# Kernel optimization log

Measured on AMD Instinct MI355X. Metric: run time of the kernel, lower is better.

Reference implementation:

```python
import jax, jax.numpy as jnp
import numpy as np

_D4_CODESZ = 4
_NUM_SCALE = 1024.0


def _code3_signs(i3, x):
    if i3 & (1 << 5):
        x[2] *= -1
    if i3 & (1 << 6):
        x[1] *= -1
    if sum(x) % 2 != 0:
        x[3] *= -1
    if i3 & (1 << 7):
        x = [-v for v in x]
    assert sum(x) % 2 == 0
    return x


def _code8_to_d4(i8):
    assert 0 <= i8 < 256
    i3 = i8 & (7 << 5)
    i8 = i8 & 31
    if i8 < 16:
        if i8 < 8:
            if i8 < 2:
                if i8 < 1:
                    return _code3_signs(i3, [0.5] * _D4_CODESZ)
                else:
                    return _code3_signs(i3, [1.5] * _D4_CODESZ)
            else:
                ibx = i8 >> 1
                if i8 & 1:
                    x = [0.5] * _D4_CODESZ
                    x[0] = 1.5
                    x[ibx] = 1.5
                else:
                    x = [1.5] * _D4_CODESZ
                    x[0] = 0.5
                    x[ibx] = 0.5
                return _code3_signs(i3, x)
        else:
            ibx = i8 & 3
            if i8 < 8 + 4:
                x = [0.5] * _D4_CODESZ
                x[ibx] = 1.5
            else:
                x = [1.5] * _D4_CODESZ
                x[ibx] = 0.5
            return _code3_signs(i3, x)
    elif i8 < 16 + 4:
        ibx = i8 & 3
        x = [0.5] * _D4_CODESZ
        x[ibx] = 2.5
        return _code3_signs(i3, x)
    else:
        ibx = i8 - 20
        ib4 = ibx & 3
        ib3 = ibx >> 2
        x = [0.5] * _D4_CODESZ
        x[ib4] = 1.5
        if ib3 >= ib4:
            ib3 += 1
        x[ib3] = 2.5
        return _code3_signs(i3, x)


def build_d4_cb():
    cb = np.zeros((256, _D4_CODESZ), dtype=np.float32)
    for i in range(256):
        cb[i] = _code8_to_d4(i)
    return jnp.asarray(cb, dtype=jnp.float16)


def fwht(x):
    """Normalized fast Walsh-Hadamard transform over the last axis (power of 2).
    The normalized Hadamard matrix is symmetric, so U and U^T coincide."""
    shp = x.shape
    n = shp[-1]
    x = x.reshape(-1, n)
    h = 1
    while h < n:
        x = x.reshape(-1, n // (2 * h), 2, h)
        a = x[:, :, 0, :]
        b = x[:, :, 1, :]
        x = jnp.stack([a + b, a - b], axis=2).reshape(-1, n)
        h *= 2
    return (x * np.float32(1.0 / np.sqrt(n))).reshape(shp)


def setup_inputs() -> dict:
    key = jax.random.key(0)
    k1, k2, k3, k4, k5 = jax.random.split(key, 5)
    m, n = 4096, 1024  # out_features=m, in_features=4*n
    d_in = _D4_CODESZ * n
    inp = {
        "input": jax.random.normal(k1, (4, 2048, d_in), dtype=jnp.float32),
        "Qidxs": jax.random.randint(k2, (m, n), 0, 256, dtype=jnp.int32),
        "SU": jnp.sign(jax.random.normal(k3, (d_in,), dtype=jnp.float32)),
        "SV": jnp.sign(jax.random.normal(k4, (m,), dtype=jnp.float32)),
        "Wscale": jax.random.uniform(k5, (1,), dtype=jnp.float32) + 0.5,
        "D4_CB": build_d4_cb(),
    }
    return inp


def reference(input, Qidxs, SU, SV, Wscale, D4_CB):
    m, n = Qidxs.shape
    d_in = _D4_CODESZ * n
    x = input.reshape(-1, d_in).astype(jnp.float32)  # [T, 4n]
    x = x * SU                                        # sign diag
    x = fwht(x)                                       # AutogradOrthoMult, transpose=1
    x = (x / _NUM_SCALE).astype(jnp.float16)
    # on-the-fly D4 dequant: gather codebook rows, fuse into GEMM
    W = D4_CB[Qidxs].reshape(m, d_in)                 # [m, 4n] fp16
    z = x @ W.T                                       # [T, m] fp16 (AutogradQuip)
    x = z.astype(jnp.float32) * (Wscale * _NUM_SCALE)
    x = fwht(x)                                       # AutogradOrthoMult, transpose=0
    x = x * SV                                        # sign diag
    return x.reshape(input.shape[:-1] + (m,))
```

## Files before the change

### kernel.cpp

```cpp
#include <hip/hip_runtime.h>
#include <hip/hip_fp16.h>

typedef _Float16 half8 __attribute__((ext_vector_type(8)));
typedef _Float16 half4v __attribute__((ext_vector_type(4)));
typedef float floatx4 __attribute__((ext_vector_type(4)));

#define K_DIM 4096
#define N_DIM 4096
#define B_ROWS 8192

#define BM 256
#define BN 256
#define BK 64
#define NTILES (K_DIM / BK)

__global__ __launch_bounds__(256) void decode_kernel(
    const int* __restrict__ qidxs, const float4* __restrict__ cb,
    half4v* __restrict__ w) {
  int i = blockIdx.x * 256 + threadIdx.x;
  float4 v = cb[qidxs[i]];
  half4v h;
  h.x = (_Float16)v.x;
  h.y = (_Float16)v.y;
  h.z = (_Float16)v.z;
  h.w = (_Float16)v.w;
  w[i] = h;
}

__global__ __launch_bounds__(256) void fwht_in_kernel(
    const float* __restrict__ x, const float* __restrict__ su,
    _Float16* __restrict__ out) {
  __shared__ float s[4096];
  const int t = threadIdx.x;
  const float4* xv = (const float4*)(x + (size_t)blockIdx.x * 4096);
  const float4* uv = (const float4*)su;
  for (int i = t; i < 1024; i += 256) {
    float4 v = xv[i], u = uv[i];
    s[4 * i + 0] = v.x * u.x;
    s[4 * i + 1] = v.y * u.y;
    s[4 * i + 2] = v.z * u.z;
    s[4 * i + 3] = v.w * u.w;
  }
  __syncthreads();
  for (int h = 1; h < 4096; h <<= 1) {
    for (int j = t; j < 2048; j += 256) {
      int idx = ((j & ~(h - 1)) << 1) | (j & (h - 1));
      float a = s[idx], b = s[idx + h];
      s[idx] = a + b;
      s[idx + h] = a - b;
    }
    __syncthreads();
  }
  const float sc = 1.0f / 65536.0f;
  half4v* ov = (half4v*)(out + (size_t)blockIdx.x * 4096);
  for (int i = t; i < 1024; i += 256) {
    half4v h4;
    h4.x = (_Float16)(s[4 * i + 0] * sc);
    h4.y = (_Float16)(s[4 * i + 1] * sc);
    h4.z = (_Float16)(s[4 * i + 2] * sc);
    h4.w = (_Float16)(s[4 * i + 3] * sc);
    ov[i] = h4;
  }
}

__device__ __forceinline__ void gload16(const _Float16* g, _Float16* l) {
  __builtin_amdgcn_global_load_lds(
      (const __attribute__((address_space(1))) void*)g,
      (__attribute__((address_space(3))) void*)l, 16, 0, 0);
}

#define MF(a, b, c) __builtin_amdgcn_mfma_f32_16x16x32_f16(a, b, c, 0, 0, 0)

#define LDA(BUFI, M, KS) \
  (*(const half8*)&sA[BUFI][wm * 128 + (M) * 16 + fr][fc ^ ((KS) << 5)])
#define LDB(BUFI, Nn, KS) \
  (*(const half8*)&sB[BUFI][wn * 64 + (Nn) * 16 + fr][fc ^ ((KS) << 5)])

#define STAGE_A(BUFI, HALF, TILE)                                            \
  {                                                                          \
    const _Float16* s_ = gA + (long)(HALF) * 128 * K_DIM + (long)(TILE)*BK;  \
    _Float16* d_ = &sA[BUFI][(HALF)*128 + sr][scl];                          \
    gload16(s_, d_);                                                         \
    gload16(s_ + 64 * (long)K_DIM, d_ + 64 * BK);                            \
  }
#define STAGE_B(BUFI, HALF, TILE)                                            \
  {                                                                          \
    const _Float16* s_ = gB + (long)(HALF) * 128 * K_DIM + (long)(TILE)*BK;  \
    _Float16* d_ = &sB[BUFI][(HALF)*128 + sr][scl];                          \
    gload16(s_, d_);                                                         \
    gload16(s_ + 64 * (long)K_DIM, d_ + 64 * BK);                            \
  }

#define WAIT4 asm volatile("s_waitcnt vmcnt(4)" ::: "memory")
#define WAIT0 asm volatile("s_waitcnt vmcnt(0)" ::: "memory")

#define PHASE(BUFI, M0, STAGE_STMT, TAIL_STMT)                               \
  {                                                                          \
    half8 x00 = LDA(BUFI, M0, 0);                                            \
    half8 x01 = LDA(BUFI, M0, 1);                                            \
    half8 x10 = LDA(BUFI, (M0) + 1, 0);                                      \
    half8 x11 = LDA(BUFI, (M0) + 1, 1);                                      \
    STAGE_STMT;                                                              \
    __builtin_amdgcn_s_barrier();                                            \
    asm volatile("s_waitcnt lgkmcnt(0)" ::: "memory");                       \
    __builtin_amdgcn_sched_barrier(0);                                       \
    __builtin_amdgcn_s_setprio(1);                                           \
    acc[M0][0] = MF(x00, bf[0][0], acc[M0][0]);                              \
    acc[M0][0] = MF(x01, bf[0][1], acc[M0][0]);                              \
    acc[M0][1] = MF(x00, bf[1][0], acc[M0][1]);                              \
    acc[M0][1] = MF(x01, bf[1][1], acc[M0][1]);                              \
    acc[M0][2] = MF(x00, bf[2][0], acc[M0][2]);                              \
    acc[M0][2] = MF(x01, bf[2][1], acc[M0][2]);                              \
    acc[M0][3] = MF(x00, bf[3][0], acc[M0][3]);                              \
    acc[M0][3] = MF(x01, bf[3][1], acc[M0][3]);                              \
    acc[(M0) + 1][0] = MF(x10, bf[0][0], acc[(M0) + 1][0]);                  \
    acc[(M0) + 1][0] = MF(x11, bf[0][1], acc[(M0) + 1][0]);                  \
    acc[(M0) + 1][1] = MF(x10, bf[1][0], acc[(M0) + 1][1]);                  \
    acc[(M0) + 1][1] = MF(x11, bf[1][1], acc[(M0) + 1][1]);                  \
    acc[(M0) + 1][2] = MF(x10, bf[2][0], acc[(M0) + 1][2]);                  \
    acc[(M0) + 1][2] = MF(x11, bf[2][1], acc[(M0) + 1][2]);                  \
    acc[(M0) + 1][3] = MF(x10, bf[3][0], acc[(M0) + 1][3]);                  \
    acc[(M0) + 1][3] = MF(x11, bf[3][1], acc[(M0) + 1][3]);                  \
    __builtin_amdgcn_s_setprio(0);                                           \
    TAIL_STMT;                                                               \
    __builtin_amdgcn_s_barrier();                                            \
  }

#define TILE(BUFI, S1, S2, S3, S4, TAILW)                                    \
  {                                                                          \
    half8 bf[4][2];                                                          \
    bf[0][0] = LDB(BUFI, 0, 0);                                              \
    bf[0][1] = LDB(BUFI, 0, 1);                                              \
    bf[1][0] = LDB(BUFI, 1, 0);                                              \
    bf[1][1] = LDB(BUFI, 1, 1);                                              \
    bf[2][0] = LDB(BUFI, 2, 0);                                              \
    bf[2][1] = LDB(BUFI, 2, 1);                                              \
    bf[3][0] = LDB(BUFI, 3, 0);                                              \
    bf[3][1] = LDB(BUFI, 3, 1);                                              \
    PHASE(BUFI, 0, S1, ;)                                                    \
    PHASE(BUFI, 2, S2, ;)                                                    \
    PHASE(BUFI, 4, S3, ;)                                                    \
    PHASE(BUFI, 6, S4, TAILW)                                                \
  }

__global__ __launch_bounds__(512) void gemm_kernel(
    const _Float16* __restrict__ A,
    const _Float16* __restrict__ B,
    float* __restrict__ C) {
  __shared__ _Float16 sA[2][BM][BK];
  __shared__ _Float16 sB[2][BN][BK];
  const int t = threadIdx.x;
  const int lane = t & 63;
  const int wave = t >> 6;
  const int wm = wave >> 2;
  const int wn = wave & 3;

  const int bid = blockIdx.x;
  const int wg = (bid & 7) * 64 + (bid >> 3);
  const long bm = (long)(wg >> 4) * BM;
  const long bn = (long)(wg & 15) * BN;

  floatx4 acc[8][4];
#pragma unroll
  for (int i = 0; i < 8; i++)
#pragma unroll
    for (int j = 0; j < 4; j++) acc[i][j] = floatx4{0.f, 0.f, 0.f, 0.f};

  const int sr = t >> 3;
  const int scl = (t & 7) << 3;
  const int sc = ((t & 7) ^ (sr & 7)) << 3;
  const _Float16* gA = A + (bm + sr) * (long)K_DIM + sc;
  const _Float16* gB = B + (bn + sr) * (long)K_DIM + sc;

  const int fr = lane & 15;
  const int fc = (((lane >> 4) ^ (lane & 7)) << 3);

  STAGE_A(0, 0, 0);
  STAGE_A(0, 1, 0);
  STAGE_B(0, 0, 0);
  STAGE_B(0, 1, 0);
  STAGE_B(1, 0, 1);
  STAGE_B(1, 1, 1);
  WAIT4;
  __builtin_amdgcn_s_barrier();

#pragma unroll 1
  for (int kt = 0; kt < NTILES - 2; kt += 2) {
    TILE(0, STAGE_A(1, 0, kt + 1), STAGE_A(1, 1, kt + 1),
         STAGE_B(0, 0, kt + 2), STAGE_B(0, 1, kt + 2), WAIT4)
    TILE(1, STAGE_A(0, 0, kt + 2), STAGE_A(0, 1, kt + 2),
         STAGE_B(1, 0, kt + 3), STAGE_B(1, 1, kt + 3), WAIT4)
  }
  TILE(0, STAGE_A(1, 0, NTILES - 1), STAGE_A(1, 1, NTILES - 1), ;, ;, WAIT0)
  TILE(1, ;, ;, ;, ;, ;)

  const int cn = lane & 15;
  const int cm4 = (lane >> 4) << 2;
#pragma unroll
  for (int m = 0; m < 8; m++) {
    const long row0 = bm + wm * 128 + m * 16 + cm4;
#pragma unroll
    for (int n = 0; n < 4; n++) {
      const long col = bn + wn * 64 + n * 16 + cn;
#pragma unroll
      for (int r = 0; r < 4; r++)
        C[(row0 + r) * (long)N_DIM + col] = (float)(_Float16)acc[m][n][r];
    }
  }
}

__global__ __launch_bounds__(256) void fwht_out_kernel(
    float* __restrict__ z, const float* __restrict__ sv,
    const float* __restrict__ wscale) {
  __shared__ float s[4096];
  const int t = threadIdx.x;
  float4* zv = (float4*)(z + (size_t)blockIdx.x * 4096);
  for (int i = t; i < 1024; i += 256) {
    float4 v = zv[i];
    s[4 * i + 0] = v.x;
    s[4 * i + 1] = v.y;
    s[4 * i + 2] = v.z;
    s[4 * i + 3] = v.w;
  }
  __syncthreads();
  for (int h = 1; h < 4096; h <<= 1) {
    for (int j = t; j < 2048; j += 256) {
      int idx = ((j & ~(h - 1)) << 1) | (j & (h - 1));
      float a = s[idx], b = s[idx + h];
      s[idx] = a + b;
      s[idx + h] = a - b;
    }
    __syncthreads();
  }
  const float sc = wscale[0] * 16.0f;
  const float4* svv = (const float4*)sv;
  for (int i = t; i < 1024; i += 256) {
    float4 u = svv[i];
    float4 o;
    o.x = s[4 * i + 0] * sc * u.x;
    o.y = s[4 * i + 1] * sc * u.y;
    o.z = s[4 * i + 2] * sc * u.z;
    o.w = s[4 * i + 3] * sc * u.w;
    zv[i] = o;
  }
}

extern "C" void kernel_launch(void* const* d_in, const int* in_sizes, int n_in,
                              void* d_out, int out_size, void* d_ws, size_t ws_size,
                              hipStream_t stream) {
  const float* input = (const float*)d_in[0];
  const int* qidxs = (const int*)d_in[1];
  const float* su = (const float*)d_in[2];
  const float* sv = (const float*)d_in[3];
  const float* wscale = (const float*)d_in[4];
  const float4* cb = (const float4*)d_in[5];
  float* out = (float*)d_out;

  if (ws_size < 100663296ull) return;
  char* ws = (char*)d_ws;
  _Float16* W16 = (_Float16*)ws;
  _Float16* Xh = (_Float16*)(ws + 33554432ull);

  decode_kernel<<<(4096 * 1024) / 256, 256, 0, stream>>>(qidxs, cb,
                                                         (half4v*)W16);
  fwht_in_kernel<<<B_ROWS, 256, 0, stream>>>(input, su, Xh);
  gemm_kernel<<<dim3((B_ROWS / BM) * (N_DIM / BN)), 512, 0, stream>>>(Xh, W16,
                                                                      out);
  fwht_out_kernel<<<B_ROWS, 256, 0, stream>>>(out, sv, wscale);
}
```

Before: 553.8 us.

## Restructure FWHT kernels as register radix-16 stages, widen decode, reorder MFMAs

Both FWHT kernels now run the 4096-point transform as three radix-16 passes. Each thread holds 16 values in registers, and data moves through an XOR-swizzled shared-memory tile between passes, so only two barriers are needed instead of twelve shared-memory butterfly stages. The decode kernel handles two codebook indices per thread and writes 16-byte vectors. The GEMM MFMA sequence is reordered so that dependent accumulations on the same accumulator are spaced apart. The aim is to cut shared-memory traffic and barrier cost in the memory-bound transform kernels, at the cost of more register use per thread.

Result: faster. 508.1 us (-8.2%).

```diff
diff --git a/kernel.cpp b/kernel.cpp
--- a/kernel.cpp
+++ b/kernel.cpp
@@ -15,52 +15,76 @@
 #define NTILES (K_DIM / BK)
 
 __global__ __launch_bounds__(256) void decode_kernel(
-    const int* __restrict__ qidxs, const float4* __restrict__ cb,
-    half4v* __restrict__ w) {
+    const int2* __restrict__ qidxs, const float4* __restrict__ cb,
+    half8* __restrict__ w) {
   int i = blockIdx.x * 256 + threadIdx.x;
-  float4 v = cb[qidxs[i]];
-  half4v h;
-  h.x = (_Float16)v.x;
-  h.y = (_Float16)v.y;
-  h.z = (_Float16)v.z;
-  h.w = (_Float16)v.w;
+  int2 q = qidxs[i];
+  float4 v0 = cb[q.x];
+  float4 v1 = cb[q.y];
+  half8 h;
+  h[0] = (_Float16)v0.x;
+  h[1] = (_Float16)v0.y;
+  h[2] = (_Float16)v0.z;
+  h[3] = (_Float16)v0.w;
+  h[4] = (_Float16)v1.x;
+  h[5] = (_Float16)v1.y;
+  h[6] = (_Float16)v1.z;
+  h[7] = (_Float16)v1.w;
   w[i] = h;
+}
+
+__device__ __forceinline__ void fwht16(float v[16]) {
+#pragma unroll
+  for (int h = 1; h < 16; h <<= 1) {
+#pragma unroll
+    for (int g = 0; g < 16; g += 2 * h) {
+#pragma unroll
+      for (int j = g; j < g + h; ++j) {
+        float a = v[j], b = v[j + h];
+        v[j] = a + b;
+        v[j + h] = a - b;
+      }
+    }
+  }
 }
 
 __global__ __launch_bounds__(256) void fwht_in_kernel(
     const float* __restrict__ x, const float* __restrict__ su,
     _Float16* __restrict__ out) {
-  __shared__ float s[4096];
+  __shared__ float s[16][264];
   const int t = threadIdx.x;
-  const float4* xv = (const float4*)(x + (size_t)blockIdx.x * 4096);
-  const float4* uv = (const float4*)su;
-  for (int i = t; i < 1024; i += 256) {
-    float4 v = xv[i], u = uv[i];
-    s[4 * i + 0] = v.x * u.x;
-    s[4 * i + 1] = v.y * u.y;
-    s[4 * i + 2] = v.z * u.z;
-    s[4 * i + 3] = v.w * u.w;
+  const float* xr = x + (size_t)blockIdx.x * 4096;
+  float v[16];
+#pragma unroll
+  for (int a = 0; a < 16; ++a) v[a] = xr[a * 256 + t] * su[a * 256 + t];
+  fwht16(v);
+  {
+    const int c = t >> 4, d = t & 15;
+    const int col = c * 16 + (d ^ c);
+#pragma unroll
+    for (int a = 0; a < 16; ++a) s[a][col] = v[a];
   }
   __syncthreads();
-  for (int h = 1; h < 4096; h <<= 1) {
-    for (int j = t; j < 2048; j += 256) {
-      int idx = ((j & ~(h - 1)) << 1) | (j & (h - 1));
-      float a = s[idx], b = s[idx + h];
-      s[idx] = a + b;
-      s[idx + h] = a - b;
-    }
-    __syncthreads();
-  }
+  const int a0 = t >> 4, d0 = t & 15;
+#pragma unroll
+  for (int c = 0; c < 16; ++c) v[c] = s[a0][c * 16 + (d0 ^ c)];
+  fwht16(v);
+#pragma unroll
+  for (int c = 0; c < 16; ++c) s[a0][c * 16 + (d0 ^ c)] = v[c];
+  __syncthreads();
+  const int c1 = t & 15;
+#pragma unroll
+  for (int d = 0; d < 16; ++d) v[d] = s[a0][c1 * 16 + (d ^ c1)];
+  fwht16(v);
   const float sc = 1.0f / 65536.0f;
-  half4v* ov = (half4v*)(out + (size_t)blockIdx.x * 4096);
-  for (int i = t; i < 1024; i += 256) {
-    half4v h4;
-    h4.x = (_Float16)(s[4 * i + 0] * sc);
-    h4.y = (_Float16)(s[4 * i + 1] * sc);
-    h4.z = (_Float16)(s[4 * i + 2] * sc);
-    h4.w = (_Float16)(s[4 * i + 3] * sc);
-    ov[i] = h4;
-  }
+  half8 h0, h1;
+#pragma unroll
+  for (int d = 0; d < 8; ++d) h0[d] = (_Float16)(v[d] * sc);
+#pragma unroll
+  for (int d = 0; d < 8; ++d) h1[d] = (_Float16)(v[d + 8] * sc);
+  half8* ov = (half8*)(out + (size_t)blockIdx.x * 4096 + t * 16);
+  ov[0] = h0;
+  ov[1] = h1;
 }
 
 __device__ __forceinline__ void gload16(const _Float16* g, _Float16* l) {
@@ -106,20 +130,20 @@
     __builtin_amdgcn_sched_barrier(0);                                       \
     __builtin_amdgcn_s_setprio(1);                                           \
     acc[M0][0] = MF(x00, bf[0][0], acc[M0][0]);                              \
+    acc[M0][1] = MF(x00, bf[1][0], acc[M0][1]);                              \
+    acc[M0][2] = MF(x00, bf[2][0], acc[M0][2]);                              \
+    acc[M0][3] = MF(x00, bf[3][0], acc[M0][3]);                              \
+    acc[(M0) + 1][0] = MF(x10, bf[0][0], acc[(M0) + 1][0]);                  \
+    acc[(M0) + 1][1] = MF(x10, bf[1][0], acc[(M0) + 1][1]);                  \
+    acc[(M0) + 1][2] = MF(x10, bf[2][0], acc[(M0) + 1][2]);                  \
+    acc[(M0) + 1][3] = MF(x10, bf[3][0], acc[(M0) + 1][3]);                  \
     acc[M0][0] = MF(x01, bf[0][1], acc[M0][0]);                              \
-    acc[M0][1] = MF(x00, bf[1][0], acc[M0][1]);                              \
     acc[M0][1] = MF(x01, bf[1][1], acc[M0][1]);                              \
-    acc[M0][2] = MF(x00, bf[2][0], acc[M0][2]);                              \
     acc[M0][2] = MF(x01, bf[2][1], acc[M0][2]);                              \
-    acc[M0][3] = MF(x00, bf[3][0], acc[M0][3]);                              \
     acc[M0][3] = MF(x01, bf[3][1], acc[M0][3]);                              \
-    acc[(M0) + 1][0] = MF(x10, bf[0][0], acc[(M0) + 1][0]);                  \
     acc[(M0) + 1][0] = MF(x11, bf[0][1], acc[(M0) + 1][0]);                  \
-    acc[(M0) + 1][1] = MF(x10, bf[1][0], acc[(M0) + 1][1]);                  \
     acc[(M0) + 1][1] = MF(x11, bf[1][1], acc[(M0) + 1][1]);                  \
-    acc[(M0) + 1][2] = MF(x10, bf[2][0], acc[(M0) + 1][2]);                  \
     acc[(M0) + 1][2] = MF(x11, bf[2][1], acc[(M0) + 1][2]);                  \
-    acc[(M0) + 1][3] = MF(x10, bf[3][0], acc[(M0) + 1][3]);                  \
     acc[(M0) + 1][3] = MF(x11, bf[3][1], acc[(M0) + 1][3]);                  \
     __builtin_amdgcn_s_setprio(0);                                           \
     TAIL_STMT;                                                               \
@@ -212,36 +236,43 @@
 __global__ __launch_bounds__(256) void fwht_out_kernel(
     float* __restrict__ z, const float* __restrict__ sv,
     const float* __restrict__ wscale) {
-  __shared__ float s[4096];
+  __shared__ float s[16][264];
   const int t = threadIdx.x;
-  float4* zv = (float4*)(z + (size_t)blockIdx.x * 4096);
-  for (int i = t; i < 1024; i += 256) {
-    float4 v = zv[i];
-    s[4 * i + 0] = v.x;
-    s[4 * i + 1] = v.y;
-    s[4 * i + 2] = v.z;
-    s[4 * i + 3] = v.w;
+  float* zr = z + (size_t)blockIdx.x * 4096;
+  float v[16];
+#pragma unroll
+  for (int a = 0; a < 16; ++a) v[a] = zr[a * 256 + t];
+  fwht16(v);
+  {
+    const int c = t >> 4, d = t & 15;
+    const int col = c * 16 + (d ^ c);
+#pragma unroll
+    for (int a = 0; a < 16; ++a) s[a][col] = v[a];
   }
   __syncthreads();
-  for (int h = 1; h < 4096; h <<= 1) {
-    for (int j = t; j < 2048; j += 256) {
-      int idx = ((j & ~(h - 1)) << 1) | (j & (h - 1));
-      float a = s[idx], b = s[idx + h];
-      s[idx] = a + b;
-      s[idx + h] = a - b;
-    }
-    __syncthreads();
-  }
-  const float sc = wscale[0] * 16.0f;
-  const float4* svv = (const float4*)sv;
-  for (int i = t; i < 1024; i += 256) {
-    float4 u = svv[i];
+  const int a0 = t >> 4, d0 = t & 15;
+#pragma unroll
+  for (int c = 0; c < 16; ++c) v[c] = s[a0][c * 16 + (d0 ^ c)];
+  fwht16(v);
+#pragma unroll
+  for (int c = 0; c < 16; ++c) s[a0][c * 16 + (d0 ^ c)] = v[c];
+  __syncthreads();
+  const int c1 = t & 15;
+#pragma unroll
+  for (int d = 0; d < 16; ++d) v[d] = s[a0][c1 * 16 + (d ^ c1)];
+  fwht16(v);
+  const float scv = wscale[0] * 16.0f;
+  const float4* svv = (const float4*)(sv + t * 16);
+  float4* zo = (float4*)(zr + t * 16);
+#pragma unroll
+  for (int q = 0; q < 4; ++q) {
+    float4 u = svv[q];
     float4 o;
-    o.x = s[4 * i + 0] * sc * u.x;
-    o.y = s[4 * i + 1] * sc * u.y;
-    o.z = s[4 * i + 2] * sc * u.z;
-    o.w = s[4 * i + 3] * sc * u.w;
-    zv[i] = o;
+    o.x = v[4 * q + 0] * scv * u.x;
+    o.y = v[4 * q + 1] * scv * u.y;
+    o.z = v[4 * q + 2] * scv * u.z;
+    o.w = v[4 * q + 3] * scv * u.w;
+    zo[q] = o;
   }
 }
 
@@ -261,8 +292,8 @@
   _Float16* W16 = (_Float16*)ws;
   _Float16* Xh = (_Float16*)(ws + 33554432ull);
 
-  decode_kernel<<<(4096 * 1024) / 256, 256, 0, stream>>>(qidxs, cb,
-                                                         (half4v*)W16);
+  decode_kernel<<<(4096 * 1024 / 2) / 256, 256, 0, stream>>>(
+      (const int2*)qidxs, cb, (half8*)W16);
   fwht_in_kernel<<<B_ROWS, 256, 0, stream>>>(input, su, Xh);
   gemm_kernel<<<dim3((B_ROWS / BM) * (N_DIM / BN)), 512, 0, stream>>>(Xh, W16,
                                                                       out);
```
